# Optimization experiments

Measured on AMD Instinct MI355X. Metric: run time of the kernel, lower is better.

## Reference

```python
import jax, jax.numpy as jnp
import numpy as np

N, E = 50000, 800000
D, DE = 128, 64
BN_EPS = 1e-5


def _bn(h, gamma, beta):
    # BatchNorm1d in training mode: biased batch statistics over the node axis
    mu = jnp.mean(h, axis=0)
    var = jnp.var(h, axis=0)
    return (h - mu) * jax.lax.rsqrt(var + BN_EPS) * gamma + beta


def setup_inputs() -> dict:
    key = jax.random.key(0)
    ks = jax.random.split(key, 12)
    s = lambda d: 1.0 / np.sqrt(d)
    return {
        "x": jax.random.normal(ks[0], (N, D), jnp.float32),
        "edge_index": jax.random.randint(ks[1], (2, E), 0, N, jnp.int64),
        "edge_attr_processed": jax.random.normal(ks[2], (E, DE), jnp.float32),
        # GINEConv edge linear: edge_dim -> node_dim
        "We": jax.random.uniform(ks[3], (D, DE), jnp.float32, -s(DE), s(DE)),
        "be": jnp.zeros((D,), jnp.float32),
        # MLP: Linear(D, 2D) -> BN(2D) -> ReLU -> Linear(2D, D)
        "W1": jax.random.uniform(ks[4], (2 * D, D), jnp.float32, -s(D), s(D)),
        "b1": jnp.zeros((2 * D,), jnp.float32),
        "g1": jnp.ones((2 * D,), jnp.float32),
        "beta1": jnp.zeros((2 * D,), jnp.float32),
        "W2": jax.random.uniform(ks[5], (D, 2 * D), jnp.float32, -s(2 * D), s(2 * D)),
        "b2": jnp.zeros((D,), jnp.float32),
        # outer BatchNorm(D)
        "g2": jnp.ones((D,), jnp.float32),
        "beta2": jnp.zeros((D,), jnp.float32),
        # GINE trainable eps (init 0.0)
        "eps": jnp.zeros((), jnp.float32),
    }


def reference(x, edge_index, edge_attr_processed, We, be, W1, b1, g1, beta1,
              W2, b2, g2, beta2, eps):
    src, dst = edge_index[0], edge_index[1]
    # GINEConv message: ReLU(x_j + Lin(edge_attr)); gather + edge add + relu
    msg = jax.nn.relu(x[src] + edge_attr_processed @ We.T + be)  # [E, D]
    # scatter-add aggregation at destination nodes
    agg = jax.ops.segment_sum(msg, dst, num_segments=x.shape[0])  # [N, D]
    h = (1.0 + eps) * x + agg
    # MLP: Linear -> BN -> ReLU -> Linear
    h = jax.nn.relu(_bn(h @ W1.T + b1, g1, beta1)) @ W2.T + b2
    # outer BN -> ReLU (dropout is identity at inference)
    return jax.nn.relu(_bn(h, g2, beta2))
```

## Files before the change

kernel.cpp:

```cpp
#include <hip/hip_runtime.h>
#include <stdint.h>
#include <stddef.h>


#define NN 50000
#define EE 800000
#define DD 128
#define DE 64
#define H1 256
#define NGRP 3125

typedef __attribute__((ext_vector_type(8))) short short8;
typedef __attribute__((ext_vector_type(4))) float floatx4;

__device__ __forceinline__ short f2bf(float f) {
    union { float f; uint32_t u; } v; v.f = f;
    return (short)((v.u + 0x7FFFu + ((v.u >> 16) & 1u)) >> 16);
}
__device__ __forceinline__ float bf2f(uint16_t u) {
    union { uint32_t u; float f; } v; v.u = (uint32_t)u << 16;
    return v.f;
}

__global__ __launch_bounds__(256) void swz_all_kernel(
    const float* __restrict__ We, const float* __restrict__ W1,
    const float* __restrict__ W2, short* __restrict__ dst) {
    int idx = blockIdx.x * 256 + threadIdx.x;
    if (idx >= 73728) return;
    const float* src; int KC, K, local; short* dp;
    if (idx < 8192)       { src = We; KC = 2; K = 64;  local = idx;          dp = dst; }
    else if (idx < 40960) { src = W1; KC = 4; K = 128; local = idx - 8192;  dp = dst + 8192; }
    else                  { src = W2; KC = 8; K = 256; local = idx - 40960; dp = dst + 40960; }
    int j = local & 7;
    int lane = (local >> 3) & 63;
    int f = local >> 9;
    int kc = f % KC;
    int nt = f / KC;
    int n = nt * 16 + (lane & 15);
    int k = kc * 32 + ((lane >> 4) & 3) * 8 + j;
    dp[local] = f2bf(src[(size_t)n * K + k]);
}

__global__ __launch_bounds__(256) void count_kernel(const int* __restrict__ ei,
                                                    uint32_t* __restrict__ deg) {
    int e = blockIdx.x * 256 + threadIdx.x;
    atomicAdd(&deg[ei[EE + e]], 1u);
}

__global__ __launch_bounds__(256) void scan1_kernel(const uint32_t* __restrict__ deg,
                                                    uint32_t* __restrict__ partial) {
    __shared__ uint32_t ls[256];
    int i = blockIdx.x * 256 + threadIdx.x;
    ls[threadIdx.x] = deg[i];
    __syncthreads();
    for (int s = 128; s > 0; s >>= 1) {
        if (threadIdx.x < s) ls[threadIdx.x] += ls[threadIdx.x + s];
        __syncthreads();
    }
    if (threadIdx.x == 0) partial[blockIdx.x] = ls[0];
}

__global__ __launch_bounds__(256) void scan2_kernel(uint32_t* __restrict__ partial) {
    __shared__ uint32_t ls[196];
    if (threadIdx.x < 196) ls[threadIdx.x] = partial[threadIdx.x];
    __syncthreads();
    if (threadIdx.x == 0) {
        uint32_t run = 0;
        for (int i = 0; i < 196; ++i) { uint32_t t = ls[i]; ls[i] = run; run += t; }
    }
    __syncthreads();
    if (threadIdx.x < 196) partial[threadIdx.x] = ls[threadIdx.x];
}

__global__ __launch_bounds__(256) void scan3_kernel(const uint32_t* __restrict__ deg,
                                                    const uint32_t* __restrict__ partial,
                                                    uint32_t* __restrict__ base,
                                                    uint32_t* __restrict__ cursor) {
    __shared__ uint32_t ls[256];
    int i = blockIdx.x * 256 + threadIdx.x;
    uint32_t v = (i < NN) ? deg[i] : 0u;
    ls[threadIdx.x] = v;
    __syncthreads();
    for (int off = 1; off < 256; off <<= 1) {
        uint32_t t = (threadIdx.x >= off) ? ls[threadIdx.x - off] : 0u;
        __syncthreads();
        ls[threadIdx.x] += t;
        __syncthreads();
    }
    if (i < NN) {
        uint32_t b = partial[blockIdx.x] + ls[threadIdx.x] - v;
        base[i] = b;
        cursor[i] = b;
    } else if (i == NN) {
        base[NN] = EE;
    }
}

__global__ __launch_bounds__(256) void pos_kernel(const int* __restrict__ ei,
                                                  uint32_t* __restrict__ cursor,
                                                  uint32_t* __restrict__ pos) {
    int e = blockIdx.x * 256 + threadIdx.x;
    pos[e] = atomicAdd(&cursor[ei[EE + e]], 1u);
}

#define EDGE_GPW 5
__global__ __launch_bounds__(256) void edge_kernel(
    const float* __restrict__ x,
    const int* __restrict__ ei,
    const float* __restrict__ ea,
    const short* __restrict__ weswz,
    const float* __restrict__ be,
    const uint32_t* __restrict__ pos,
    uint16_t* __restrict__ msg)
{
    __shared__ uint16_t tile[4][16 * 132];
    const int wave = threadIdx.x >> 6;
    const int lane = threadIdx.x & 63;
    const int l16 = lane & 15;
    const int q = lane >> 4;

    const short8* wp = (const short8*)weswz;
    short8 bfr[16];
#pragma unroll
    for (int f = 0; f < 16; ++f) bfr[f] = wp[f * 64 + lane];
    float bev[8];
#pragma unroll
    for (int t = 0; t < 8; ++t) bev[t] = be[t * 16 + l16];

    const int gbase = (blockIdx.x * 4 + wave) * EDGE_GPW;
    for (int g = 0; g < EDGE_GPW; ++g) {
        const int e0 = (gbase + g) * 16;
        const float* earow = ea + (size_t)(e0 + l16) * DE + q * 8;
        floatx4 p0 = *(const floatx4*)(earow);
        floatx4 p1 = *(const floatx4*)(earow + 4);
        floatx4 p2 = *(const floatx4*)(earow + 32);
        floatx4 p3 = *(const floatx4*)(earow + 36);
        short8 af0, af1;
#pragma unroll
        for (int j = 0; j < 4; ++j) {
            af0[j]     = f2bf(p0[j]);
            af0[j + 4] = f2bf(p1[j]);
            af1[j]     = f2bf(p2[j]);
            af1[j + 4] = f2bf(p3[j]);
        }
        floatx4 acc[8];
#pragma unroll
        for (int t = 0; t < 8; ++t) {
            floatx4 z = {0.f, 0.f, 0.f, 0.f};
            z = __builtin_amdgcn_mfma_f32_16x16x32_bf16(af0, bfr[t * 2], z, 0, 0, 0);
            acc[t] = __builtin_amdgcn_mfma_f32_16x16x32_bf16(af1, bfr[t * 2 + 1], z, 0, 0, 0);
        }
#pragma unroll
        for (int r = 0; r < 4; ++r) {
            const int e = e0 + q * 4 + r;
            const int s = ei[e];
            const float* xr = x + (size_t)s * DD;
#pragma unroll
            for (int t = 0; t < 8; ++t) {
                float v = fmaxf(acc[t][r] + bev[t] + xr[t * 16 + l16], 0.f);
                tile[wave][(q * 4 + r) * 132 + t * 16 + l16] = (uint16_t)f2bf(v);
            }
        }
        __asm__ volatile("s_waitcnt lgkmcnt(0)" ::: "memory");
#pragma unroll
        for (int p = 0; p < 4; ++p) {
            const int row = p * 4 + q;
            const uint32_t pp = pos[e0 + row];
            uint4 val = *(const uint4*)&tile[wave][row * 132 + l16 * 8];
            *(uint4*)(msg + (size_t)pp * DD + l16 * 8) = val;
        }
        __asm__ volatile("s_waitcnt vmcnt(0)" ::: "memory");
    }
}

__global__ __launch_bounds__(256) void reduce_kernel(
    const uint16_t* __restrict__ msg,
    const uint32_t* __restrict__ basep,
    const float* __restrict__ x,
    const float* __restrict__ epsp,
    uint16_t* __restrict__ hbf)
{
    const int n = blockIdx.x * 4 + (threadIdx.x >> 6);
    const int lane = threadIdx.x & 63;
    const uint32_t b0 = basep[n];
    const uint32_t d = basep[n + 1] - b0;
    const uint32_t* mp = (const uint32_t*)msg + (size_t)b0 * 64 + lane;
    float s0a = 0.f, s1a = 0.f, s0b = 0.f, s1b = 0.f;
    float s0c = 0.f, s1c = 0.f, s0d = 0.f, s1d = 0.f;
    uint32_t i = 0;
    for (; i + 4 <= d; i += 4) {
        uint32_t u0 = mp[(size_t)(i + 0) * 64];
        uint32_t u1 = mp[(size_t)(i + 1) * 64];
        uint32_t u2 = mp[(size_t)(i + 2) * 64];
        uint32_t u3 = mp[(size_t)(i + 3) * 64];
        s0a += bf2f((uint16_t)(u0 & 0xFFFFu)); s1a += bf2f((uint16_t)(u0 >> 16));
        s0b += bf2f((uint16_t)(u1 & 0xFFFFu)); s1b += bf2f((uint16_t)(u1 >> 16));
        s0c += bf2f((uint16_t)(u2 & 0xFFFFu)); s1c += bf2f((uint16_t)(u2 >> 16));
        s0d += bf2f((uint16_t)(u3 & 0xFFFFu)); s1d += bf2f((uint16_t)(u3 >> 16));
    }
    for (; i < d; ++i) {
        uint32_t u = mp[(size_t)i * 64];
        s0a += bf2f((uint16_t)(u & 0xFFFFu)); s1a += bf2f((uint16_t)(u >> 16));
    }
    float s0 = (s0a + s0b) + (s0c + s0d);
    float s1 = (s1a + s1b) + (s1c + s1d);
    const float c1 = 1.0f + epsp[0];
    const int idx = n * DD + lane * 2;
    float2 xv = *(const float2*)(x + idx);
    uint32_t pk = (uint32_t)(uint16_t)f2bf(c1 * xv.x + s0) |
                  ((uint32_t)(uint16_t)f2bf(c1 * xv.y + s1) << 16);
    ((uint32_t*)hbf)[idx >> 1] = pk;
}

__global__ __launch_bounds__(256) void gemm1_kernel(
    const uint16_t* __restrict__ hbf,
    const short* __restrict__ w1swz,
    const float* __restrict__ b1,
    uint16_t* __restrict__ t1,
    float* __restrict__ gsum,
    float* __restrict__ gsq)
{
    __shared__ float ls[H1];
    __shared__ float ls2[H1];
    const int tid = threadIdx.x;
    ls[tid] = 0.f; ls2[tid] = 0.f;
    __syncthreads();

    const int wave = tid >> 6;
    const int lane = tid & 63;
    const int l16 = lane & 15;
    const int q = lane >> 4;
    const short8* wp = (const short8*)w1swz;

    const int grp = blockIdx.x * 4 + wave;
    if (grp < NGRP) {
        const int n0 = grp * 16;
        const uint16_t* hr = hbf + (size_t)(n0 + l16) * DD + q * 8;
        short8 af[4];
#pragma unroll
        for (int kc = 0; kc < 4; ++kc) af[kc] = *(const short8*)(hr + kc * 32);
#pragma unroll
        for (int nt = 0; nt < 16; ++nt) {
            floatx4 acc = {0.f, 0.f, 0.f, 0.f};
#pragma unroll
            for (int kc = 0; kc < 4; ++kc)
                acc = __builtin_amdgcn_mfma_f32_16x16x32_bf16(
                    af[kc], wp[(nt * 4 + kc) * 64 + lane], acc, 0, 0, 0);
            const float bb = b1[nt * 16 + l16];
            float s = 0.f, s2 = 0.f;
#pragma unroll
            for (int r = 0; r < 4; ++r) {
                float v = acc[r] + bb;
                t1[(size_t)(n0 + q * 4 + r) * H1 + nt * 16 + l16] = (uint16_t)f2bf(v);
                s += v; s2 += v * v;
            }
            atomicAdd(&ls[nt * 16 + l16], s);
            atomicAdd(&ls2[nt * 16 + l16], s2);
        }
    }
    __syncthreads();
    atomicAdd(&gsum[tid], ls[tid]);
    atomicAdd(&gsq[tid], ls2[tid]);
}

__global__ __launch_bounds__(256) void gemm2_kernel(
    const uint16_t* __restrict__ t1,
    const float* __restrict__ scale1,
    const float* __restrict__ shift1,
    const short* __restrict__ w2swz,
    const float* __restrict__ b2,
    uint16_t* __restrict__ h2,
    float* __restrict__ gsum,
    float* __restrict__ gsq)
{
    __shared__ float ls[DD];
    __shared__ float ls2[DD];
    const int tid = threadIdx.x;
    if (tid < DD) { ls[tid] = 0.f; ls2[tid] = 0.f; }
    __syncthreads();

    const int wave = tid >> 6;
    const int lane = tid & 63;
    const int l16 = lane & 15;
    const int q = lane >> 4;
    const short8* wp = (const short8*)w2swz;

    const int grp = blockIdx.x * 4 + wave;
    if (grp < NGRP) {
        const int n0 = grp * 16;
        const uint16_t* tr = t1 + (size_t)(n0 + l16) * H1 + q * 8;
        floatx4 acc[8];
#pragma unroll
        for (int nt = 0; nt < 8; ++nt) acc[nt] = (floatx4){0.f, 0.f, 0.f, 0.f};
#pragma unroll
        for (int kc = 0; kc < 8; ++kc) {
            short8 tv = *(const short8*)(tr + kc * 32);
            const int kb = kc * 32 + q * 8;
            short8 af;
#pragma unroll
            for (int j = 0; j < 8; ++j) {
                float u = bf2f((uint16_t)tv[j]) * scale1[kb + j] + shift1[kb + j];
                af[j] = f2bf(fmaxf(u, 0.f));
            }
#pragma unroll
            for (int nt = 0; nt < 8; ++nt)
                acc[nt] = __builtin_amdgcn_mfma_f32_16x16x32_bf16(
                    af, wp[(nt * 8 + kc) * 64 + lane], acc[nt], 0, 0, 0);
        }
#pragma unroll
        for (int nt = 0; nt < 8; ++nt) {
            const float bb = b2[nt * 16 + l16];
            float s = 0.f, s2 = 0.f;
#pragma unroll
            for (int r = 0; r < 4; ++r) {
                float v = acc[nt][r] + bb;
                h2[(size_t)(n0 + q * 4 + r) * DD + nt * 16 + l16] = (uint16_t)f2bf(v);
                s += v; s2 += v * v;
            }
            atomicAdd(&ls[nt * 16 + l16], s);
            atomicAdd(&ls2[nt * 16 + l16], s2);
        }
    }
    __syncthreads();
    if (tid < DD) {
        atomicAdd(&gsum[tid], ls[tid]);
        atomicAdd(&gsq[tid], ls2[tid]);
    }
}

__global__ void finalize_kernel(const float* __restrict__ ssum,
                                const float* __restrict__ ssumsq,
                                const float* __restrict__ gamma,
                                const float* __restrict__ beta,
                                float* __restrict__ scale,
                                float* __restrict__ shift, int C) {
    int c = threadIdx.x;
    if (c >= C) return;
    float mu = ssum[c] * (1.0f / NN);
    float var = ssumsq[c] * (1.0f / NN) - mu * mu;
    float rs = rsqrtf(var + 1e-5f);
    float sc = gamma[c] * rs;
    scale[c] = sc;
    shift[c] = beta[c] - mu * sc;
}

__global__ __launch_bounds__(256) void out_kernel(const uint16_t* __restrict__ h2,
                                                  const float* __restrict__ scale2,
                                                  const float* __restrict__ shift2,
                                                  float* __restrict__ out) {
    int idx = blockIdx.x * 256 + threadIdx.x;
    int base = idx * 8;
    int c = base & (DD - 1);
    uint4 pk = *(const uint4*)(h2 + base);
    const uint32_t u[4] = {pk.x, pk.y, pk.z, pk.w};
    floatx4 o0, o1;
#pragma unroll
    for (int j = 0; j < 4; ++j) {
        float vlo = bf2f((uint16_t)(u[j] & 0xFFFFu));
        float vhi = bf2f((uint16_t)(u[j] >> 16));
        int cc = c + j * 2;
        float a = fmaxf(vlo * scale2[cc] + shift2[cc], 0.f);
        float b = fmaxf(vhi * scale2[cc + 1] + shift2[cc + 1], 0.f);
        if (j < 2) { o0[j * 2] = a; o0[j * 2 + 1] = b; }
        else       { o1[(j - 2) * 2] = a; o1[(j - 2) * 2 + 1] = b; }
    }
    *(floatx4*)(out + base) = o0;
    *(floatx4*)(out + base + 4) = o1;
}

extern "C" void kernel_launch(void* const* d_in, const int* in_sizes, int n_in,
                              void* d_out, int out_size, void* d_ws, size_t ws_size,
                              hipStream_t stream) {
    const float* x     = (const float*)d_in[0];
    const int*   ei    = (const int*)d_in[1];
    const float* ea    = (const float*)d_in[2];
    const float* We    = (const float*)d_in[3];
    const float* be    = (const float*)d_in[4];
    const float* W1    = (const float*)d_in[5];
    const float* b1    = (const float*)d_in[6];
    const float* g1    = (const float*)d_in[7];
    const float* beta1 = (const float*)d_in[8];
    const float* W2    = (const float*)d_in[9];
    const float* b2    = (const float*)d_in[10];
    const float* g2    = (const float*)d_in[11];
    const float* beta2 = (const float*)d_in[12];
    const float* epsp  = (const float*)d_in[13];

    float* ws      = (float*)d_ws;
    float* gsum1   = ws + 0;
    float* gsq1    = ws + 256;
    float* gsum2   = ws + 512;
    float* gsq2    = ws + 640;
    float* scale1  = ws + 768;
    float* shift1  = ws + 1024;
    float* scale2  = ws + 1280;
    float* shift2  = ws + 1408;
    uint32_t* deg     = (uint32_t*)(ws + 1536);
    uint32_t* basep   = deg + 50176;
    uint32_t* cursor  = basep + 50432;
    uint32_t* partial = cursor + 50176;
    uint32_t* pos     = partial + 256;
    uint16_t* hbf     = (uint16_t*)(pos + EE);
    uint16_t* msg     = hbf + (size_t)NN * DD;
    uint16_t* t1      = msg;
    uint16_t* h2      = t1 + (size_t)NN * H1;
    short*    wswz    = (short*)(msg + (size_t)EE * DD);
    short*    weswz   = wswz;
    short*    w1swz   = wswz + 8192;
    short*    w2swz   = wswz + 40960;

    hipMemsetAsync(ws, 0, (1536 + 50176) * sizeof(uint32_t), stream);

    swz_all_kernel<<<dim3(288), 256, 0, stream>>>(We, W1, W2, wswz);
    count_kernel<<<dim3(3125), 256, 0, stream>>>(ei, deg);
    scan1_kernel<<<dim3(196), 256, 0, stream>>>(deg, partial);
    scan2_kernel<<<dim3(1), 256, 0, stream>>>(partial);
    scan3_kernel<<<dim3(196), 256, 0, stream>>>(deg, partial, basep, cursor);
    pos_kernel<<<dim3(3125), 256, 0, stream>>>(ei, cursor, pos);

    edge_kernel<<<dim3(2500), 256, 0, stream>>>(x, ei, ea, weswz, be, pos, msg);
    reduce_kernel<<<dim3(12500), 256, 0, stream>>>(msg, basep, x, epsp, hbf);

    gemm1_kernel<<<dim3(782), 256, 0, stream>>>(hbf, w1swz, b1, t1, gsum1, gsq1);
    finalize_kernel<<<dim3(1), 256, 0, stream>>>(gsum1, gsq1, g1, beta1, scale1, shift1, H1);

    gemm2_kernel<<<dim3(782), 256, 0, stream>>>(t1, scale1, shift1, w2swz, b2, h2, gsum2, gsq2);
    finalize_kernel<<<dim3(1), 128, 0, stream>>>(gsum2, gsq2, g2, beta2, scale2, shift2, DD);

    out_kernel<<<dim3(3125), 256, 0, stream>>>(h2, scale2, shift2, (float*)d_out);
}
```

Baseline: 627.2 us.

## Write edge messages in permuted feature order directly from registers, skipping LDS staging

The edge kernel no longer stages each 16-edge message tile in shared memory. Each lane packs its MFMA outputs into a 16-byte store laid out in a permuted feature order. The permutation is undone downstream: the reduce kernel reads x at the matching permuted offsets, and W1 is swizzled with the same column permutation, so gemm1 still consumes consistent data. This removes the LDS round-trip and its wait barriers, and hoists the index and position loads, at the cost of a less intuitive layout that three kernels must keep in sync.

```diff
diff --git a/kernel.cpp b/kernel.cpp
--- a/kernel.cpp
+++ b/kernel.cpp
@@ -27,9 +27,9 @@
     const float* __restrict__ W2, short* __restrict__ dst) {
     int idx = blockIdx.x * 256 + threadIdx.x;
     if (idx >= 73728) return;
-    const float* src; int KC, K, local; short* dp;
+    const float* src; int KC, K, local; short* dp; bool perm = false;
     if (idx < 8192)       { src = We; KC = 2; K = 64;  local = idx;          dp = dst; }
-    else if (idx < 40960) { src = W1; KC = 4; K = 128; local = idx - 8192;  dp = dst + 8192; }
+    else if (idx < 40960) { src = W1; KC = 4; K = 128; local = idx - 8192;  dp = dst + 8192; perm = true; }
     else                  { src = W2; KC = 8; K = 256; local = idx - 40960; dp = dst + 40960; }
     int j = local & 7;
     int lane = (local >> 3) & 63;
@@ -38,6 +38,7 @@
     int nt = f / KC;
     int n = nt * 16 + (lane & 15);
     int k = kc * 32 + ((lane >> 4) & 3) * 8 + j;
+    if (perm) k = ((k & 7) << 4) | (k >> 3);
     dp[local] = f2bf(src[(size_t)n * K + k]);
 }
 
@@ -113,7 +114,6 @@
     const uint32_t* __restrict__ pos,
     uint16_t* __restrict__ msg)
 {
-    __shared__ uint16_t tile[4][16 * 132];
     const int wave = threadIdx.x >> 6;
     const int lane = threadIdx.x & 63;
     const int l16 = lane & 15;
@@ -150,26 +150,26 @@
             z = __builtin_amdgcn_mfma_f32_16x16x32_bf16(af0, bfr[t * 2], z, 0, 0, 0);
             acc[t] = __builtin_amdgcn_mfma_f32_16x16x32_bf16(af1, bfr[t * 2 + 1], z, 0, 0, 0);
         }
+        int   sidx[4];
+        uint32_t ppv[4];
 #pragma unroll
         for (int r = 0; r < 4; ++r) {
-            const int e = e0 + q * 4 + r;
-            const int s = ei[e];
-            const float* xr = x + (size_t)s * DD;
-#pragma unroll
-            for (int t = 0; t < 8; ++t) {
-                float v = fmaxf(acc[t][r] + bev[t] + xr[t * 16 + l16], 0.f);
-                tile[wave][(q * 4 + r) * 132 + t * 16 + l16] = (uint16_t)f2bf(v);
+            sidx[r] = ei[e0 + q * 4 + r];
+            ppv[r]  = pos[e0 + q * 4 + r];
+        }
+#pragma unroll
+        for (int r = 0; r < 4; ++r) {
+            const float* xr = x + (size_t)sidx[r] * DD + l16;
+            uint32_t pk[4];
+#pragma unroll
+            for (int tt = 0; tt < 4; ++tt) {
+                float v0 = fmaxf(acc[2 * tt][r]     + bev[2 * tt]     + xr[(2 * tt) * 16], 0.f);
+                float v1 = fmaxf(acc[2 * tt + 1][r] + bev[2 * tt + 1] + xr[(2 * tt + 1) * 16], 0.f);
+                pk[tt] = (uint32_t)(uint16_t)f2bf(v0) | ((uint32_t)(uint16_t)f2bf(v1) << 16);
             }
-        }
-        __asm__ volatile("s_waitcnt lgkmcnt(0)" ::: "memory");
-#pragma unroll
-        for (int p = 0; p < 4; ++p) {
-            const int row = p * 4 + q;
-            const uint32_t pp = pos[e0 + row];
-            uint4 val = *(const uint4*)&tile[wave][row * 132 + l16 * 8];
-            *(uint4*)(msg + (size_t)pp * DD + l16 * 8) = val;
-        }
-        __asm__ volatile("s_waitcnt vmcnt(0)" ::: "memory");
+            uint4 val = {pk[0], pk[1], pk[2], pk[3]};
+            *(uint4*)(msg + (size_t)ppv[r] * DD + l16 * 8) = val;
+        }
     }
 }
 
@@ -205,11 +205,13 @@
     float s0 = (s0a + s0b) + (s0c + s0d);
     float s1 = (s1a + s1b) + (s1c + s1d);
     const float c1 = 1.0f + epsp[0];
-    const int idx = n * DD + lane * 2;
-    float2 xv = *(const float2*)(x + idx);
-    uint32_t pk = (uint32_t)(uint16_t)f2bf(c1 * xv.x + s0) |
-                  ((uint32_t)(uint16_t)f2bf(c1 * xv.y + s1) << 16);
-    ((uint32_t*)hbf)[idx >> 1] = pk;
+    const int o0 = (((lane * 2) & 7) << 4) + (lane >> 2);
+    const float* xrow = x + (size_t)n * DD;
+    float xa = xrow[o0];
+    float xb = xrow[o0 + 16];
+    uint32_t pk = (uint32_t)(uint16_t)f2bf(c1 * xa + s0) |
+                  ((uint32_t)(uint16_t)f2bf(c1 * xb + s1) << 16);
+    ((uint32_t*)hbf)[n * 64 + lane] = pk;
 }
 
 __global__ __launch_bounds__(256) void gemm1_kernel(
```

Result: faster. 613.7 us (-2.1%).

## Fuse edge message and CSR reduction into one kernel with LDS accumulation

Applied to the files above, without the earlier changes.

Replaces the separate edge kernel, which wrote bf16 messages to a large scattered buffer, and the reduce kernel, which read them back, with one fused kernel. Each wave walks the dst-sorted edges of 8 consecutive nodes and accumulates ReLU messages into per-node LDS rows with shared-memory atomics. A scatter kernel now writes the sorted source index and original edge id instead of a position array, and the We swizzle is permuted so each lane owns 8 contiguous output features, allowing vectorized x gathers. This removes the E×D message round trip through global memory, at the cost of LDS atomics and indirect, less coalesced reads of edge_attr.

```diff
diff --git a/kernel.cpp b/kernel.cpp
--- a/kernel.cpp
+++ b/kernel.cpp
@@ -9,6 +9,9 @@
 #define DE 64
 #define H1 256
 #define NGRP 3125
+#define NPW 8
+#define LROW 132
+#define NROW 9
 
 typedef __attribute__((ext_vector_type(8))) short short8;
 typedef __attribute__((ext_vector_type(4))) float floatx4;
@@ -27,8 +30,8 @@
     const float* __restrict__ W2, short* __restrict__ dst) {
     int idx = blockIdx.x * 256 + threadIdx.x;
     if (idx >= 73728) return;
-    const float* src; int KC, K, local; short* dp;
-    if (idx < 8192)       { src = We; KC = 2; K = 64;  local = idx;          dp = dst; }
+    const float* src; int KC, K, local; short* dp; bool efeat = false;
+    if (idx < 8192)       { src = We; KC = 2; K = 64;  local = idx;          dp = dst; efeat = true; }
     else if (idx < 40960) { src = W1; KC = 4; K = 128; local = idx - 8192;  dp = dst + 8192; }
     else                  { src = W2; KC = 8; K = 256; local = idx - 40960; dp = dst + 40960; }
     int j = local & 7;
@@ -36,7 +39,7 @@
     int f = local >> 9;
     int kc = f % KC;
     int nt = f / KC;
-    int n = nt * 16 + (lane & 15);
+    int n = efeat ? ((lane & 15) * 8 + nt) : (nt * 16 + (lane & 15));
     int k = kc * 32 + ((lane >> 4) & 3) * 8 + j;
     dp[local] = f2bf(src[(size_t)n * K + k]);
 }
@@ -96,45 +99,89 @@
     }
 }
 
-__global__ __launch_bounds__(256) void pos_kernel(const int* __restrict__ ei,
-                                                  uint32_t* __restrict__ cursor,
-                                                  uint32_t* __restrict__ pos) {
+__global__ __launch_bounds__(256) void scat_kernel(const int* __restrict__ ei,
+                                                   uint32_t* __restrict__ cursor,
+                                                   int* __restrict__ esrc,
+                                                   uint32_t* __restrict__ eorg) {
     int e = blockIdx.x * 256 + threadIdx.x;
-    pos[e] = atomicAdd(&cursor[ei[EE + e]], 1u);
-}
-
-#define EDGE_GPW 5
-__global__ __launch_bounds__(256) void edge_kernel(
+    uint32_t p = atomicAdd(&cursor[ei[EE + e]], 1u);
+    esrc[p] = ei[e];
+    eorg[p] = (uint32_t)e;
+}
+
+__global__ __launch_bounds__(256) void fused_kernel(
     const float* __restrict__ x,
-    const int* __restrict__ ei,
+    const uint32_t* __restrict__ basep,
+    const int* __restrict__ esrc,
+    const uint32_t* __restrict__ eorg,
     const float* __restrict__ ea,
     const short* __restrict__ weswz,
     const float* __restrict__ be,
-    const uint32_t* __restrict__ pos,
-    uint16_t* __restrict__ msg)
+    const float* __restrict__ epsp,
+    uint16_t* __restrict__ hbf)
 {
-    __shared__ uint16_t tile[4][16 * 132];
+    __shared__ float lacc[4][NROW * LROW];
     const int wave = threadIdx.x >> 6;
     const int lane = threadIdx.x & 63;
     const int l16 = lane & 15;
     const int q = lane >> 4;
+    float* my = lacc[wave];
+
+    const int wid = blockIdx.x * 4 + wave;
+    const int n0 = wid * NPW;
+    if (n0 >= NN) return;
+
+#pragma unroll
+    for (int k = 0; k < NROW * LROW; k += 64) {
+        int kk = k + lane;
+        if (kk < NROW * LROW) my[kk] = 0.f;
+    }
 
     const short8* wp = (const short8*)weswz;
     short8 bfr[16];
 #pragma unroll
     for (int f = 0; f < 16; ++f) bfr[f] = wp[f * 64 + lane];
-    float bev[8];
-#pragma unroll
-    for (int t = 0; t < 8; ++t) bev[t] = be[t * 16 + l16];
-
-    const int gbase = (blockIdx.x * 4 + wave) * EDGE_GPW;
-    for (int g = 0; g < EDGE_GPW; ++g) {
-        const int e0 = (gbase + g) * 16;
-        const float* earow = ea + (size_t)(e0 + l16) * DE + q * 8;
+    floatx4 bv0 = *(const floatx4*)(be + l16 * 8);
+    floatx4 bv1 = *(const floatx4*)(be + l16 * 8 + 4);
+
+    uint32_t bpk[NPW + 1];
+#pragma unroll
+    for (int k = 0; k <= NPW; ++k) {
+        int nk = n0 + k; if (nk > NN) nk = NN;
+        bpk[k] = basep[nk];
+    }
+    const uint32_t eb = bpk[0], ee2 = bpk[NPW];
+
+    __asm__ volatile("s_waitcnt lgkmcnt(0)" ::: "memory");
+
+    uint32_t org = eorg[min(eb + (uint32_t)l16, (uint32_t)(EE - 1))];
+    int srcv[4];
+#pragma unroll
+    for (int r = 0; r < 4; ++r)
+        srcv[r] = esrc[min(eb + (uint32_t)(q * 4 + r), (uint32_t)(EE - 1))];
+
+    for (uint32_t i = eb; i < ee2; i += 16) {
+        const float* earow = ea + (size_t)org * DE + q * 8;
         floatx4 p0 = *(const floatx4*)(earow);
         floatx4 p1 = *(const floatx4*)(earow + 4);
         floatx4 p2 = *(const floatx4*)(earow + 32);
         floatx4 p3 = *(const floatx4*)(earow + 36);
+        floatx4 xa[4], xb[4];
+#pragma unroll
+        for (int r = 0; r < 4; ++r) {
+            const float* xr = x + (size_t)srcv[r] * DD + l16 * 8;
+            xa[r] = *(const floatx4*)(xr);
+            xb[r] = *(const floatx4*)(xr + 4);
+        }
+        uint32_t orgN = org; int srcN[4];
+#pragma unroll
+        for (int r = 0; r < 4; ++r) srcN[r] = srcv[r];
+        if (i + 16 < ee2) {
+            orgN = eorg[min(i + 16u + (uint32_t)l16, (uint32_t)(EE - 1))];
+#pragma unroll
+            for (int r = 0; r < 4; ++r)
+                srcN[r] = esrc[min(i + 16u + (uint32_t)(q * 4 + r), (uint32_t)(EE - 1))];
+        }
         short8 af0, af1;
 #pragma unroll
         for (int j = 0; j < 4; ++j) {
@@ -152,64 +199,46 @@
         }
 #pragma unroll
         for (int r = 0; r < 4; ++r) {
-            const int e = e0 + q * 4 + r;
-            const int s = ei[e];
-            const float* xr = x + (size_t)s * DD;
+            const uint32_t idx = i + (uint32_t)(q * 4 + r);
+            int nl = 0;
+#pragma unroll
+            for (int k = 1; k <= NPW; ++k) nl += (idx >= bpk[k]) ? 1 : 0;
+            float* bl = my + nl * LROW + l16 * 8;
 #pragma unroll
             for (int t = 0; t < 8; ++t) {
-                float v = fmaxf(acc[t][r] + bev[t] + xr[t * 16 + l16], 0.f);
-                tile[wave][(q * 4 + r) * 132 + t * 16 + l16] = (uint16_t)f2bf(v);
+                float xv = (t < 4) ? xa[r][t] : xb[r][t - 4];
+                float bvv = (t < 4) ? bv0[t] : bv1[t - 4];
+                float v = fmaxf(acc[t][r] + bvv + xv, 0.f);
+                atomicAdd(bl + t, v);
             }
         }
-        __asm__ volatile("s_waitcnt lgkmcnt(0)" ::: "memory");
-#pragma unroll
-        for (int p = 0; p < 4; ++p) {
-            const int row = p * 4 + q;
-            const uint32_t pp = pos[e0 + row];
-            uint4 val = *(const uint4*)&tile[wave][row * 132 + l16 * 8];
-            *(uint4*)(msg + (size_t)pp * DD + l16 * 8) = val;
-        }
-        __asm__ volatile("s_waitcnt vmcnt(0)" ::: "memory");
-    }
-}
-
-__global__ __launch_bounds__(256) void reduce_kernel(
-    const uint16_t* __restrict__ msg,
-    const uint32_t* __restrict__ basep,
-    const float* __restrict__ x,
-    const float* __restrict__ epsp,
-    uint16_t* __restrict__ hbf)
-{
-    const int n = blockIdx.x * 4 + (threadIdx.x >> 6);
-    const int lane = threadIdx.x & 63;
-    const uint32_t b0 = basep[n];
-    const uint32_t d = basep[n + 1] - b0;
-    const uint32_t* mp = (const uint32_t*)msg + (size_t)b0 * 64 + lane;
-    float s0a = 0.f, s1a = 0.f, s0b = 0.f, s1b = 0.f;
-    float s0c = 0.f, s1c = 0.f, s0d = 0.f, s1d = 0.f;
-    uint32_t i = 0;
-    for (; i + 4 <= d; i += 4) {
-        uint32_t u0 = mp[(size_t)(i + 0) * 64];
-        uint32_t u1 = mp[(size_t)(i + 1) * 64];
-        uint32_t u2 = mp[(size_t)(i + 2) * 64];
-        uint32_t u3 = mp[(size_t)(i + 3) * 64];
-        s0a += bf2f((uint16_t)(u0 & 0xFFFFu)); s1a += bf2f((uint16_t)(u0 >> 16));
-        s0b += bf2f((uint16_t)(u1 & 0xFFFFu)); s1b += bf2f((uint16_t)(u1 >> 16));
-        s0c += bf2f((uint16_t)(u2 & 0xFFFFu)); s1c += bf2f((uint16_t)(u2 >> 16));
-        s0d += bf2f((uint16_t)(u3 & 0xFFFFu)); s1d += bf2f((uint16_t)(u3 >> 16));
-    }
-    for (; i < d; ++i) {
-        uint32_t u = mp[(size_t)i * 64];
-        s0a += bf2f((uint16_t)(u & 0xFFFFu)); s1a += bf2f((uint16_t)(u >> 16));
-    }
-    float s0 = (s0a + s0b) + (s0c + s0d);
-    float s1 = (s1a + s1b) + (s1c + s1d);
-    const float c1 = 1.0f + epsp[0];
-    const int idx = n * DD + lane * 2;
-    float2 xv = *(const float2*)(x + idx);
-    uint32_t pk = (uint32_t)(uint16_t)f2bf(c1 * xv.x + s0) |
-                  ((uint32_t)(uint16_t)f2bf(c1 * xv.y + s1) << 16);
-    ((uint32_t*)hbf)[idx >> 1] = pk;
+        org = orgN;
+#pragma unroll
+        for (int r = 0; r < 4; ++r) srcv[r] = srcN[r];
+    }
+
+    __asm__ volatile("s_waitcnt lgkmcnt(0)" ::: "memory");
+    const int nl = lane >> 3;
+    const int s = lane & 7;
+    const int n = n0 + nl;
+    if (n < NN) {
+        const float c1 = 1.0f + epsp[0];
+        const float* ar = my + nl * LROW + s * 16;
+        const float* xr = x + (size_t)n * DD + s * 16;
+        uint32_t pk[8];
+#pragma unroll
+        for (int w = 0; w < 4; ++w) {
+            floatx4 av = *(const floatx4*)(ar + w * 4);
+            floatx4 xv = *(const floatx4*)(xr + w * 4);
+            pk[w * 2]     = (uint32_t)(uint16_t)f2bf(c1 * xv[0] + av[0]) |
+                            ((uint32_t)(uint16_t)f2bf(c1 * xv[1] + av[1]) << 16);
+            pk[w * 2 + 1] = (uint32_t)(uint16_t)f2bf(c1 * xv[2] + av[2]) |
+                            ((uint32_t)(uint16_t)f2bf(c1 * xv[3] + av[3]) << 16);
+        }
+        uint16_t* op = hbf + (size_t)n * DD + s * 16;
+        *(uint4*)(op)     = (uint4){pk[0], pk[1], pk[2], pk[3]};
+        *(uint4*)(op + 8) = (uint4){pk[4], pk[5], pk[6], pk[7]};
+    }
 }
 
 __global__ __launch_bounds__(256) void gemm1_kernel(
@@ -399,12 +428,12 @@
     uint32_t* basep   = deg + 50176;
     uint32_t* cursor  = basep + 50432;
     uint32_t* partial = cursor + 50176;
-    uint32_t* pos     = partial + 256;
-    uint16_t* hbf     = (uint16_t*)(pos + EE);
-    uint16_t* msg     = hbf + (size_t)NN * DD;
-    uint16_t* t1      = msg;
+    int*      esrc    = (int*)(partial + 256);
+    uint32_t* eorg    = (uint32_t*)(esrc + EE);
+    uint16_t* hbf     = (uint16_t*)(eorg + EE);
+    uint16_t* t1      = hbf + (size_t)NN * DD;
     uint16_t* h2      = t1 + (size_t)NN * H1;
-    short*    wswz    = (short*)(msg + (size_t)EE * DD);
+    short*    wswz    = (short*)(h2 + (size_t)NN * DD);
     short*    weswz   = wswz;
     short*    w1swz   = wswz + 8192;
     short*    w2swz   = wswz + 40960;
@@ -416,10 +445,10 @@
     scan1_kernel<<<dim3(196), 256, 0, stream>>>(deg, partial);
     scan2_kernel<<<dim3(1), 256, 0, stream>>>(partial);
     scan3_kernel<<<dim3(196), 256, 0, stream>>>(deg, partial, basep, cursor);
-    pos_kernel<<<dim3(3125), 256, 0, stream>>>(ei, cursor, pos);
-
-    edge_kernel<<<dim3(2500), 256, 0, stream>>>(x, ei, ea, weswz, be, pos, msg);
-    reduce_kernel<<<dim3(12500), 256, 0, stream>>>(msg, basep, x, epsp, hbf);
+    scat_kernel<<<dim3(3125), 256, 0, stream>>>(ei, cursor, esrc, eorg);
+
+    fused_kernel<<<dim3(1563), 256, 0, stream>>>(x, basep, esrc, eorg, ea,
+                                                 weswz, be, epsp, hbf);
 
     gemm1_kernel<<<dim3(782), 256, 0, stream>>>(hbf, w1swz, b1, t1, gsum1, gsq1);
     finalize_kernel<<<dim3(1), 256, 0, stream>>>(gsum1, gsq1, g1, beta1, scale1, shift1, H1);
```

After: 1.075 ms. 1.71x slower.
